# Kernel tuning notes

Hardware: AMD Instinct MI355X
Metric: run time of the kernel (lower is better)

## Reference

```python
import jax, jax.numpy as jnp
import numpy as np

X_MIN, X_MAX = -2.0, 2.0


def _pchip_slopes_uniform(y, h):
    # y: [..., K], uniform knot spacing h. Fritsch-Carlson / PCHIP slopes.
    delta = (y[..., 1:] - y[..., :-1]) / h            # [..., K-1]
    dp, dn = delta[..., :-1], delta[..., 1:]          # [..., K-2]
    same_sign = dp * dn > 0
    d_mid = jnp.where(same_sign, 2.0 * dp * dn / (dp + dn + 1e-12), 0.0)

    def _fix_endpoint(d_end, delta0, delta1):
        d_end = jnp.where(d_end * delta0 <= 0, 0.0, d_end)
        d_end = jnp.where((delta0 * delta1 < 0) & (jnp.abs(d_end) > 3.0 * jnp.abs(delta0)),
                          3.0 * delta0, d_end)
        return d_end

    d0 = _fix_endpoint((3.0 * delta[..., 0] - delta[..., 1]) / 2.0, delta[..., 0], delta[..., 1])
    dN = _fix_endpoint((3.0 * delta[..., -1] - delta[..., -2]) / 2.0, delta[..., -1], delta[..., -2])
    return jnp.concatenate([d0[..., None], d_mid, dN[..., None]], axis=-1)


def setup_inputs() -> dict:
    key = jax.random.key(0)
    k1, k2 = jax.random.split(key)
    B, O, D, K = 8192, 64, 64, 64
    x = jax.random.normal(k1, (B, D), dtype=jnp.float32)
    coeffs = 0.01 * jax.random.normal(k2, (O, D, K), dtype=jnp.float32)
    bias = jnp.zeros((O,), dtype=jnp.float32)
    return {"x": x, "coeffs": coeffs, "bias": bias}


def reference(x, coeffs, bias):
    # x: [B, D]; coeffs: [O, D, K]; bias: [O] -> out: [B, O]
    O, D, K = coeffs.shape
    h = (X_MAX - X_MIN) / (K - 1)
    slopes = _pchip_slopes_uniform(coeffs, h)          # [O, D, K]

    t = (x - X_MIN) / h                                # [B, D]
    idx = jnp.clip(jnp.floor(t).astype(jnp.int32), 0, K - 2)
    u = (t - idx)[None]                                # [1, B, D]

    darange = jnp.arange(D)[None, :]                   # broadcasts with idx [B, D]
    y0 = coeffs[:, darange, idx]                       # [O, B, D]
    y1 = coeffs[:, darange, idx + 1]
    d0 = slopes[:, darange, idx]
    d1 = slopes[:, darange, idx + 1]

    u2 = u * u
    u3 = u2 * u
    h00 = 2.0 * u3 - 3.0 * u2 + 1.0
    h10 = u3 - 2.0 * u2 + u
    h01 = -2.0 * u3 + 3.0 * u2
    h11 = u3 - u2
    interp = h00 * y0 + h10 * (h * d0) + h01 * y1 + h11 * (h * d1)  # [O, B, D]

    # linear extrapolation outside [X_MIN, X_MAX]
    left = coeffs[:, :, 0][:, None, :] + slopes[:, :, 0][:, None, :] * (x - X_MIN)[None]
    right = coeffs[:, :, -1][:, None, :] + slopes[:, :, -1][:, None, :] * (x - X_MAX)[None]
    interp = jnp.where((x < X_MIN)[None], left, interp)
    interp = jnp.where((x > X_MAX)[None], right, interp)

    out = interp.sum(axis=-1).T + bias[None, :]        # [B, O]
    return out
```

## Files before the change

### kernel.cpp

```cpp
#include <hip/hip_runtime.h>
#include <hip/hip_fp16.h>
#include <stdint.h>


typedef _Float16 half2v __attribute__((ext_vector_type(2)));

#if defined(__has_builtin)
#if __has_builtin(__builtin_amdgcn_fdot2)
#define HAS_FDOT2 1
#endif
#endif

__device__ __forceinline__ uint32_t h16(float f) {
    return (uint32_t)__half_as_ushort(__float2half(f));
}

__device__ __forceinline__ float dot2acc(uint32_t a_bits, uint32_t b_bits, float acc) {
    half2v a = __builtin_bit_cast(half2v, a_bits);
    half2v b = __builtin_bit_cast(half2v, b_bits);
#ifdef HAS_FDOT2
    return __builtin_amdgcn_fdot2(a, b, acc, false);
#else
    return acc + (float)a.x * (float)b.x + (float)a.y * (float)b.y;
#endif
}

__global__ void build_table(const float* __restrict__ coeffs, uint2* __restrict__ T) {
    const float hf = 4.0f / 63.0f;
    const float inv_hf = 63.0f / 4.0f;
    int d  = blockIdx.x >> 2;
    int ob = (blockIdx.x & 3) << 4;
    __shared__ float Y[16][65];
    int t = threadIdx.x;
    {
        int ol = t >> 4;
        int k4 = (t & 15) << 2;
        const float* src = coeffs + (size_t)(ob + ol) * 4096 + d * 64 + k4;
        float4 v = *(const float4*)src;
        Y[ol][k4 + 0] = v.x; Y[ol][k4 + 1] = v.y;
        Y[ol][k4 + 2] = v.z; Y[ol][k4 + 3] = v.w;
    }
    __syncthreads();
    for (int c = t; c < 1024; c += 256) {
        int ol = c & 15;
        int i  = c >> 4;
        const float* Yr = Y[ol];
        auto delt = [&](int k) -> float { return (Yr[k + 1] - Yr[k]) * inv_hf; };
        auto endslope = [&](float a, float b) -> float {
            float de = (3.0f * a - b) * 0.5f;
            de = (de * a <= 0.0f) ? 0.0f : de;
            de = ((a * b < 0.0f) && (fabsf(de) > 3.0f * fabsf(a))) ? 3.0f * a : de;
            return de;
        };
        auto slope = [&](int k) -> float {
            if (k == 0)  return endslope(delt(0), delt(1));
            if (k == 63) return endslope(delt(62), delt(61));
            float dp = delt(k - 1), dn = delt(k);
            return (dp * dn > 0.0f) ? (2.0f * dp * dn) / (dp + dn + 1e-12f) : 0.0f;
        };
        uint2 pk;
        if (i < 63) {
            float y0 = Yr[i], y1 = Yr[i + 1];
            float di = slope(i), dj = slope(i + 1);
            float c0 = y0;
            float c1 = hf * di;
            float c2 = 3.0f * (y1 - y0) - hf * (2.0f * di + dj);
            float c3 = 2.0f * (y0 - y1) + hf * (di + dj);
            pk.x = (h16(c1) << 16) | h16(c0);
            pk.y = (h16(c3) << 16) | h16(c2);
        } else {
            float yN = Yr[63];
            float dN = slope(63);
            pk.x = (h16(hf * dN) << 16) | h16(yN);
            pk.y = 0u;
        }
        T[(size_t)d * 4096 + i * 64 + (ob + ol)] = pk;
    }
}

__global__ void __launch_bounds__(256) kan_main(const float* __restrict__ x,
                                                const float* __restrict__ bias,
                                                const char* __restrict__ Tb,
                                                float* __restrict__ out) {
    int t    = threadIdx.x;
    int lane = t & 63;
    int wv   = t >> 6;
    int b    = blockIdx.x * 4 + wv;

    uint32_t ra, rb, roff;
    {
        float xv = x[b * 64 + lane];
        float tt = (xv + 2.0f) * 15.75f;
        int i = (int)floorf(tt);
        i = i < 0 ? 0 : (i > 62 ? 62 : i);
        float u = tt - (float)i;
        float w1, w2, w3; uint32_t off;
        if (xv < -2.0f)      { w1 = tt;          w2 = 0.f;    w3 = 0.f;    off = 0u; }
        else if (xv > 2.0f)  { w1 = tt - 63.0f;  w2 = 0.f;    w3 = 0.f;    off = 63u << 9; }
        else                 { w1 = u;           w2 = u * u;  w3 = w2 * u; off = (uint32_t)i << 9; }
        ra   = (h16(w1) << 16) | 0x3C00u;
        rb   = (h16(w3) << 16) | h16(w2);
        roff = ((uint32_t)lane << 15) | off;
    }

    float acc0 = bias[lane];
    float acc1 = 0.0f;
    int laneoff = lane << 3;
    #pragma unroll
    for (int d = 0; d < 64; ++d) {
        uint32_t off = (uint32_t)__builtin_amdgcn_readlane((int)roff, d);
        uint32_t wa  = (uint32_t)__builtin_amdgcn_readlane((int)ra,   d);
        uint32_t wb  = (uint32_t)__builtin_amdgcn_readlane((int)rb,   d);
        uint2 c = *(const uint2*)(Tb + off + laneoff);
        acc0 = dot2acc(wa, c.x, acc0);
        acc1 = dot2acc(wb, c.y, acc1);
    }
    out[b * 64 + lane] = acc0 + acc1;
}

extern "C" void kernel_launch(void* const* d_in, const int* in_sizes, int n_in,
                              void* d_out, int out_size, void* d_ws, size_t ws_size,
                              hipStream_t stream) {
    const float* x      = (const float*)d_in[0];
    const float* coeffs = (const float*)d_in[1];
    const float* bias   = (const float*)d_in[2];
    float* out = (float*)d_out;

    uint2* T = (uint2*)d_ws;
    build_table<<<dim3(256), dim3(256), 0, stream>>>(coeffs, T);
    kan_main<<<dim3(2048), dim3(256), 0, stream>>>(x, bias, (const char*)d_ws, out);
}
```

Baseline: 78.74 us.

## Split D across blocks with LDS-staged table slices and a separate reduction pass

```diff
diff --git a/kernel.cpp b/kernel.cpp
--- a/kernel.cpp
+++ b/kernel.cpp
@@ -8,6 +8,9 @@
 #if defined(__has_builtin)
 #if __has_builtin(__builtin_amdgcn_fdot2)
 #define HAS_FDOT2 1
+#endif
+#if __has_builtin(__builtin_amdgcn_global_load_lds)
+#define HAS_GLL 1
 #endif
 #endif
 
@@ -78,44 +81,94 @@
     }
 }
 
-__global__ void __launch_bounds__(256) kan_main(const float* __restrict__ x,
-                                                const float* __restrict__ bias,
+__device__ __forceinline__ void stage_slice(const char* __restrict__ gsrc,
+                                            uint2* __restrict__ ldst, int t) {
+#ifdef HAS_GLL
+    typedef const __attribute__((address_space(1))) uint32_t* gp_t;
+    typedef __attribute__((address_space(3))) uint32_t* lp_t;
+    char* l = (char*)ldst;
+    #pragma unroll
+    for (int k = 0; k < 8; ++k) {
+        __builtin_amdgcn_global_load_lds((gp_t)(gsrc + k * 4096 + t * 16),
+                                         (lp_t)(l + k * 4096 + t * 16), 16, 0, 0);
+    }
+#else
+    const uint4* g = (const uint4*)gsrc;
+    uint4* l = (uint4*)ldst;
+    #pragma unroll
+    for (int k = 0; k < 8; ++k) l[k * 256 + t] = g[k * 256 + t];
+#endif
+}
+
+__global__ void __launch_bounds__(256) kan_part(const float* __restrict__ x,
                                                 const char* __restrict__ Tb,
-                                                float* __restrict__ out) {
+                                                float* __restrict__ partial) {
+    __shared__ uint2 buf[2][4096];
     int t    = threadIdx.x;
     int lane = t & 63;
-    int wv   = t >> 6;
-    int b    = blockIdx.x * 4 + wv;
+    int w    = t >> 6;
+    int bs   = blockIdx.x & 31;
+    int dp   = blockIdx.x >> 5;
+    int b    = bs * 256 + t;
 
-    uint32_t ra, rb, roff;
+    uint32_t rwa[4], rwb[4], roff[4];
     {
-        float xv = x[b * 64 + lane];
-        float tt = (xv + 2.0f) * 15.75f;
-        int i = (int)floorf(tt);
-        i = i < 0 ? 0 : (i > 62 ? 62 : i);
-        float u = tt - (float)i;
-        float w1, w2, w3; uint32_t off;
-        if (xv < -2.0f)      { w1 = tt;          w2 = 0.f;    w3 = 0.f;    off = 0u; }
-        else if (xv > 2.0f)  { w1 = tt - 63.0f;  w2 = 0.f;    w3 = 0.f;    off = 63u << 9; }
-        else                 { w1 = u;           w2 = u * u;  w3 = w2 * u; off = (uint32_t)i << 9; }
-        ra   = (h16(w1) << 16) | 0x3C00u;
-        rb   = (h16(w3) << 16) | h16(w2);
-        roff = ((uint32_t)lane << 15) | off;
+        float4 xv4 = *(const float4*)(x + (size_t)b * 64 + dp * 4);
+        float xs[4] = {xv4.x, xv4.y, xv4.z, xv4.w};
+        #pragma unroll
+        for (int j = 0; j < 4; ++j) {
+            float xv = xs[j];
+            float tt = (xv + 2.0f) * 15.75f;
+            int i = (int)floorf(tt);
+            i = i < 0 ? 0 : (i > 62 ? 62 : i);
+            float u = tt - (float)i;
+            float w1, w2, w3; uint32_t off;
+            if (xv < -2.0f)      { w1 = tt;         w2 = 0.f;   w3 = 0.f;    off = 0u; }
+            else if (xv > 2.0f)  { w1 = tt - 63.0f; w2 = 0.f;   w3 = 0.f;    off = 63u << 9; }
+            else                 { w1 = u;          w2 = u * u; w3 = w2 * u; off = (uint32_t)i << 9; }
+            rwa[j]  = (h16(w1) << 16) | 0x3C00u;
+            rwb[j]  = (h16(w3) << 16) | h16(w2);
+            roff[j] = off;
+        }
     }
 
-    float acc0 = bias[lane];
-    float acc1 = 0.0f;
+    float acc[64];
+    #pragma unroll
+    for (int bb = 0; bb < 64; ++bb) acc[bb] = 0.0f;
+
+    stage_slice(Tb + (size_t)(dp * 4 + 0) * 32768, buf[0], t);
+    __syncthreads();
+
     int laneoff = lane << 3;
     #pragma unroll
-    for (int d = 0; d < 64; ++d) {
-        uint32_t off = (uint32_t)__builtin_amdgcn_readlane((int)roff, d);
-        uint32_t wa  = (uint32_t)__builtin_amdgcn_readlane((int)ra,   d);
-        uint32_t wb  = (uint32_t)__builtin_amdgcn_readlane((int)rb,   d);
-        uint2 c = *(const uint2*)(Tb + off + laneoff);
-        acc0 = dot2acc(wa, c.x, acc0);
-        acc1 = dot2acc(wb, c.y, acc1);
+    for (int j = 0; j < 4; ++j) {
+        if (j < 3)
+            stage_slice(Tb + (size_t)(dp * 4 + j + 1) * 32768, buf[(j + 1) & 1], t);
+        const char* sl = (const char*)buf[j & 1];
+        #pragma unroll
+        for (int bb = 0; bb < 64; ++bb) {
+            uint32_t off = (uint32_t)__builtin_amdgcn_readlane((int)roff[j], bb);
+            uint32_t wa  = (uint32_t)__builtin_amdgcn_readlane((int)rwa[j],  bb);
+            uint32_t wb  = (uint32_t)__builtin_amdgcn_readlane((int)rwb[j],  bb);
+            uint2 c = *(const uint2*)(sl + off + laneoff);
+            acc[bb] = dot2acc(wb, c.y, dot2acc(wa, c.x, acc[bb]));
+        }
+        __syncthreads();
     }
-    out[b * 64 + lane] = acc0 + acc1;
+
+    float* pbase = partial + ((size_t)dp * 8192 + bs * 256 + w * 64) * 64 + lane;
+    #pragma unroll
+    for (int bb = 0; bb < 64; ++bb) pbase[bb * 64] = acc[bb];
+}
+
+__global__ void __launch_bounds__(256) kan_reduce(const float* __restrict__ partial,
+                                                  const float* __restrict__ bias,
+                                                  float* __restrict__ out) {
+    int id = blockIdx.x * 256 + threadIdx.x;
+    float s = bias[id & 63];
+    #pragma unroll
+    for (int p = 0; p < 16; ++p) s += partial[(size_t)p * 524288 + id];
+    out[id] = s;
 }
 
 extern "C" void kernel_launch(void* const* d_in, const int* in_sizes, int n_in,
@@ -126,7 +179,10 @@
     const float* bias   = (const float*)d_in[2];
     float* out = (float*)d_out;
 
-    uint2* T = (uint2*)d_ws;
+    uint2* T       = (uint2*)d_ws;
+    float* partial = (float*)((char*)d_ws + (4u << 20));
+
     build_table<<<dim3(256), dim3(256), 0, stream>>>(coeffs, T);
-    kan_main<<<dim3(2048), dim3(256), 0, stream>>>(x, bias, (const char*)d_ws, out);
+    kan_part<<<dim3(512), dim3(256), 0, stream>>>(x, (const char*)d_ws, partial);
+    kan_reduce<<<dim3(2048), dim3(256), 0, stream>>>(partial, bias, out);
 }
```

Measured after the change: 97.80 us. 24.2% more time.
